# Kernel tuning notes

Measured on AMD Instinct MI355X. Metric: run time of the kernel, lower is better.

## Reference

```python
import jax, jax.numpy as jnp
import numpy as np
import math


def setup_inputs() -> dict:
    key = jax.random.key(0)
    k1, k2, k3 = jax.random.split(key, 3)
    B, L, H, E = 2, 2048, 8, 64
    queries = jax.random.normal(k1, (B, L, H, E), dtype=jnp.float32)
    keys = jax.random.normal(k2, (B, L, H, E), dtype=jnp.float32)
    values = jax.random.normal(k3, (B, L, H, E), dtype=jnp.float32)
    return {"queries": queries, "keys": keys, "values": values}


def reference(queries, keys, values):
    B, L, H, E = queries.shape
    scale = 1.0 / math.sqrt(E)
    # [B,H,L,S] attention scores
    scores = jnp.einsum('blhe,bshe->bhls', queries, keys)
    # causal mask: positions s > l masked to -inf (scale * -inf stays -inf)
    causal = jnp.triu(jnp.ones((L, L), dtype=bool), k=1)  # True above diagonal
    scores = jnp.where(causal[None, None, :, :], -jnp.inf, scores)
    attn = scale * scores
    SA = jax.nn.softmax(attn, axis=-1)  # dropout p=0.0 -> identity
    V = jnp.einsum('bhls,bshd->blhd', SA, values)
    return (V, SA)
```

## Files before the change

### kernel.cpp

```cpp
#include <hip/hip_runtime.h>
#include <math.h>

#define L_DIM 2048
#define H_DIM 8
#define ROWSTRIDE 512
#define NT 512
#define QSCALE 0.18033688011112042f

typedef __attribute__((ext_vector_type(8))) short short8;
typedef __attribute__((ext_vector_type(4))) float floatx4;

__device__ __forceinline__ unsigned short f2bf(float f) {
    unsigned int u = __builtin_bit_cast(unsigned int, f);
    return (unsigned short)((u + 0x8000u) >> 16);
}

__device__ __forceinline__ float fexp2(float x) {
#if __has_builtin(__builtin_amdgcn_exp2f)
    return __builtin_amdgcn_exp2f(x);
#else
    return exp2f(x);
#endif
}

__global__ __launch_bounds__(NT, 4)
void attn_mfma2(const float* __restrict__ Q, const float* __restrict__ K,
                const float* __restrict__ Vv, float* __restrict__ outV,
                float* __restrict__ outSA)
{
    __shared__ __align__(16) unsigned char smem[65536];
    unsigned short* Qs = (unsigned short*)(smem);
    unsigned short* Ks = (unsigned short*)(smem + 9216);
    unsigned short* Vt = (unsigned short*)(smem + 27648);
    unsigned short* Ps = (unsigned short*)(smem + 46080);
    float* Ml = (float*)(smem + 64512);
    float* Ll = (float*)(smem + 65024);
    float* Ob = (float*)(smem + 9216);

    const int t   = threadIdx.x;
    const int g   = t >> 8;
    const int u   = t & 255;
    const int bid = blockIdx.x;
    const int idx = bid & 31;
    const int qt  = (idx & 1) ? (31 - (idx >> 1)) : (idx >> 1);
    const int bh  = bid >> 5;
    const int h   = bh & 7;
    const int b   = bh >> 3;
    const int q0  = qt << 6;

    const int lane = t & 63;
    const int wg   = (t >> 6) & 3;
    const int l15  = lane & 15;
    const int quad = lane >> 4;

    const float* Qb = Q  + (size_t)b * L_DIM * ROWSTRIDE + h * 64;
    const float* Kb = K  + (size_t)b * L_DIM * ROWSTRIDE + h * 64;
    const float* Vb = Vv + (size_t)b * L_DIM * ROWSTRIDE + h * 64;
    float* saBase = outSA + (size_t)(b * H_DIM + h) * L_DIM * L_DIM;

    {
        const int sr = t >> 3, se = (t & 7) * 8;
        const float* src = Qb + (size_t)(q0 + sr) * ROWSTRIDE + se;
        float4 f0 = *(const float4*)(src);
        float4 f1 = *(const float4*)(src + 4);
        union { unsigned short us[8]; short8 v; } p;
        p.us[0] = f2bf(f0.x * QSCALE); p.us[1] = f2bf(f0.y * QSCALE);
        p.us[2] = f2bf(f0.z * QSCALE); p.us[3] = f2bf(f0.w * QSCALE);
        p.us[4] = f2bf(f1.x * QSCALE); p.us[5] = f2bf(f1.y * QSCALE);
        p.us[6] = f2bf(f1.z * QSCALE); p.us[7] = f2bf(f1.w * QSCALE);
        *(short8*)&Qs[sr * 72 + se] = p.v;
    }
    __syncthreads();

    const short8 aQ0 = *(const short8*)&Qs[(16 * wg + l15) * 72 + quad * 8];
    const short8 aQ1 = *(const short8*)&Qs[(16 * wg + l15) * 72 + 32 + quad * 8];

    const int ntiles = qt + 1;
    const int niter  = (ntiles + 1) >> 1;
    const int ksr = u >> 2, kse = (u & 3) * 16;
    unsigned short* myKs = Ks + g * 4608;
    unsigned short* myVt = Vt + g * 4608;
    unsigned short* myPs = Ps + g * 4608;

    float m_r[4], l_r[4];
#pragma unroll
    for (int r = 0; r < 4; ++r) { m_r[r] = -INFINITY; l_r[r] = 0.f; }

    for (int it = 0; it < niter; ++it) {
        const int st = 2 * it + g;
        const bool active = (st < ntiles);
        const int s0 = st << 6;
        __syncthreads();
        if (active) {
            const float* src = Kb + (size_t)(s0 + ksr) * ROWSTRIDE + kse;
            float4 f0 = *(const float4*)(src + 0);
            float4 f1 = *(const float4*)(src + 4);
            float4 f2 = *(const float4*)(src + 8);
            float4 f3 = *(const float4*)(src + 12);
            union { unsigned short us[8]; short8 v; } p0, p1;
            p0.us[0]=f2bf(f0.x); p0.us[1]=f2bf(f0.y); p0.us[2]=f2bf(f0.z); p0.us[3]=f2bf(f0.w);
            p0.us[4]=f2bf(f1.x); p0.us[5]=f2bf(f1.y); p0.us[6]=f2bf(f1.z); p0.us[7]=f2bf(f1.w);
            p1.us[0]=f2bf(f2.x); p1.us[1]=f2bf(f2.y); p1.us[2]=f2bf(f2.z); p1.us[3]=f2bf(f2.w);
            p1.us[4]=f2bf(f3.x); p1.us[5]=f2bf(f3.y); p1.us[6]=f2bf(f3.z); p1.us[7]=f2bf(f3.w);
            *(short8*)&myKs[ksr * 72 + kse]     = p0.v;
            *(short8*)&myKs[ksr * 72 + kse + 8] = p1.v;
        }
        __syncthreads();
        if (!active) continue;

        floatx4 d[4];
#pragma unroll
        for (int j = 0; j < 4; ++j) {
            short8 b0 = *(const short8*)&myKs[(16 * j + l15) * 72 + quad * 8];
            short8 b1 = *(const short8*)&myKs[(16 * j + l15) * 72 + 32 + quad * 8];
            floatx4 acc = {0.f, 0.f, 0.f, 0.f};
            acc = __builtin_amdgcn_mfma_f32_16x16x32_bf16(aQ0, b0, acc, 0, 0, 0);
            acc = __builtin_amdgcn_mfma_f32_16x16x32_bf16(aQ1, b1, acc, 0, 0, 0);
            d[j] = acc;
        }
        const bool diag = (st == qt);
#pragma unroll
        for (int r = 0; r < 4; ++r) {
            const int lrow = q0 + 16 * wg + quad * 4 + r;
            float v0 = d[0][r], v1 = d[1][r], v2 = d[2][r], v3 = d[3][r];
            if (diag) {
                v0 = (s0 +  0 + l15 <= lrow) ? v0 : -INFINITY;
                v1 = (s0 + 16 + l15 <= lrow) ? v1 : -INFINITY;
                v2 = (s0 + 32 + l15 <= lrow) ? v2 : -INFINITY;
                v3 = (s0 + 48 + l15 <= lrow) ? v3 : -INFINITY;
            }
            float vm = fmaxf(fmaxf(v0, v1), fmaxf(v2, v3));
#pragma unroll
            for (int mk = 1; mk < 16; mk <<= 1) vm = fmaxf(vm, __shfl_xor(vm, mk));
            const float mnew = fmaxf(m_r[r], vm);
            float es = fexp2(v0 - mnew) + fexp2(v1 - mnew) +
                       fexp2(v2 - mnew) + fexp2(v3 - mnew);
#pragma unroll
            for (int mk = 1; mk < 16; mk <<= 1) es += __shfl_xor(es, mk);
            l_r[r] = l_r[r] * fexp2(m_r[r] - mnew) + es;
            m_r[r] = mnew;
        }
    }

    __syncthreads();
    if (l15 == 0) {
#pragma unroll
        for (int r = 0; r < 4; ++r) {
            const int row = 16 * wg + quad * 4 + r;
            Ml[g * 64 + row] = m_r[r];
            Ll[g * 64 + row] = l_r[r];
        }
    }
    __syncthreads();
    float mfin[4], invl[4];
#pragma unroll
    for (int r = 0; r < 4; ++r) {
        const int row = 16 * wg + quad * 4 + r;
        float m0 = Ml[row], m1 = Ml[64 + row];
        float l0 = Ll[row], l1 = Ll[64 + row];
        float mf = fmaxf(m0, m1);
        float lf = l0 * fexp2(m0 - mf) + l1 * fexp2(m1 - mf);
        mfin[r] = mf;
        invl[r] = 1.0f / lf;
    }

    floatx4 oacc[4];
#pragma unroll
    for (int j = 0; j < 4; ++j) oacc[j] = (floatx4){0.f, 0.f, 0.f, 0.f};

    for (int it = 0; it < niter; ++it) {
        const int st = 2 * it + g;
        const bool active = (st < ntiles);
        const int s0 = st << 6;
        __syncthreads();
        if (active) {
            {
                const float* src = Kb + (size_t)(s0 + ksr) * ROWSTRIDE + kse;
                float4 f0 = *(const float4*)(src + 0);
                float4 f1 = *(const float4*)(src + 4);
                float4 f2 = *(const float4*)(src + 8);
                float4 f3 = *(const float4*)(src + 12);
                union { unsigned short us[8]; short8 v; } p0, p1;
                p0.us[0]=f2bf(f0.x); p0.us[1]=f2bf(f0.y); p0.us[2]=f2bf(f0.z); p0.us[3]=f2bf(f0.w);
                p0.us[4]=f2bf(f1.x); p0.us[5]=f2bf(f1.y); p0.us[6]=f2bf(f1.z); p0.us[7]=f2bf(f1.w);
                p1.us[0]=f2bf(f2.x); p1.us[1]=f2bf(f2.y); p1.us[2]=f2bf(f2.z); p1.us[3]=f2bf(f2.w);
                p1.us[4]=f2bf(f3.x); p1.us[5]=f2bf(f3.y); p1.us[6]=f2bf(f3.z); p1.us[7]=f2bf(f3.w);
                *(short8*)&myKs[ksr * 72 + kse]     = p0.v;
                *(short8*)&myKs[ksr * 72 + kse + 8] = p1.v;
            }
            {
                const float* src = Vb + (size_t)(s0 + ksr) * ROWSTRIDE + kse;
                float4 f0 = *(const float4*)(src + 0);
                float4 f1 = *(const float4*)(src + 4);
                float4 f2 = *(const float4*)(src + 8);
                float4 f3 = *(const float4*)(src + 12);
                myVt[(kse +  0) * 72 + ksr] = f2bf(f0.x);
                myVt[(kse +  1) * 72 + ksr] = f2bf(f0.y);
                myVt[(kse +  2) * 72 + ksr] = f2bf(f0.z);
                myVt[(kse +  3) * 72 + ksr] = f2bf(f0.w);
                myVt[(kse +  4) * 72 + ksr] = f2bf(f1.x);
                myVt[(kse +  5) * 72 + ksr] = f2bf(f1.y);
                myVt[(kse +  6) * 72 + ksr] = f2bf(f1.z);
                myVt[(kse +  7) * 72 + ksr] = f2bf(f1.w);
                myVt[(kse +  8) * 72 + ksr] = f2bf(f2.x);
                myVt[(kse +  9) * 72 + ksr] = f2bf(f2.y);
                myVt[(kse + 10) * 72 + ksr] = f2bf(f2.z);
                myVt[(kse + 11) * 72 + ksr] = f2bf(f2.w);
                myVt[(kse + 12) * 72 + ksr] = f2bf(f3.x);
                myVt[(kse + 13) * 72 + ksr] = f2bf(f3.y);
                myVt[(kse + 14) * 72 + ksr] = f2bf(f3.z);
                myVt[(kse + 15) * 72 + ksr] = f2bf(f3.w);
            }
        }
        __syncthreads();
        if (!active) continue;

        floatx4 d[4];
#pragma unroll
        for (int j = 0; j < 4; ++j) {
            short8 b0 = *(const short8*)&myKs[(16 * j + l15) * 72 + quad * 8];
            short8 b1 = *(const short8*)&myKs[(16 * j + l15) * 72 + 32 + quad * 8];
            floatx4 acc = {0.f, 0.f, 0.f, 0.f};
            acc = __builtin_amdgcn_mfma_f32_16x16x32_bf16(aQ0, b0, acc, 0, 0, 0);
            acc = __builtin_amdgcn_mfma_f32_16x16x32_bf16(aQ1, b1, acc, 0, 0, 0);
            d[j] = acc;
        }
        const bool diag = (st == qt);
#pragma unroll
        for (int r = 0; r < 4; ++r) {
            const int lrow = q0 + 16 * wg + quad * 4 + r;
            float* sap = saBase + (size_t)lrow * L_DIM + s0 + l15;
            const float mr = mfin[r], il = invl[r];
#pragma unroll
            for (int j = 0; j < 4; ++j) {
                float v = d[j][r];
                bool ok = !diag || (s0 + 16 * j + l15 <= lrow);
                float p = ok ? fexp2(v - mr) * il : 0.0f;
                sap[16 * j] = p;
                myPs[(16 * wg + quad * 4 + r) * 72 + 16 * j + l15] = f2bf(p);
            }
        }
        short8 aP0 = *(const short8*)&myPs[(16 * wg + l15) * 72 + quad * 8];
        short8 aP1 = *(const short8*)&myPs[(16 * wg + l15) * 72 + 32 + quad * 8];
#pragma unroll
        for (int j = 0; j < 4; ++j) {
            short8 bv0 = *(const short8*)&myVt[(16 * j + l15) * 72 + quad * 8];
            short8 bv1 = *(const short8*)&myVt[(16 * j + l15) * 72 + 32 + quad * 8];
            oacc[j] = __builtin_amdgcn_mfma_f32_16x16x32_bf16(aP0, bv0, oacc[j], 0, 0, 0);
            oacc[j] = __builtin_amdgcn_mfma_f32_16x16x32_bf16(aP1, bv1, oacc[j], 0, 0, 0);
        }
    }

    __syncthreads();
    if (g == 1) {
#pragma unroll
        for (int r = 0; r < 4; ++r) {
            const int row = 16 * wg + quad * 4 + r;
#pragma unroll
            for (int j = 0; j < 4; ++j)
                Ob[row * 65 + 16 * j + l15] = oacc[j][r];
        }
    }
    __syncthreads();
    if (g == 0) {
#pragma unroll
        for (int r = 0; r < 4; ++r) {
            const int row = 16 * wg + quad * 4 + r;
            float* op = outV + ((size_t)b * L_DIM + q0 + row) * ROWSTRIDE + h * 64 + l15;
#pragma unroll
            for (int j = 0; j < 4; ++j)
                op[16 * j] = oacc[j][r] + Ob[row * 65 + 16 * j + l15];
        }
    }

    {
        const int z0 = ntiles << 6;
        const int zr = t >> 3;
        float* rowp = saBase + (size_t)(q0 + zr) * L_DIM;
        const float4 zf = {0.f, 0.f, 0.f, 0.f};
        for (int s = z0 + (t & 7) * 4; s < L_DIM; s += 32)
            *(float4*)(rowp + s) = zf;
    }
}

extern "C" void kernel_launch(void* const* d_in, const int* in_sizes, int n_in,
                              void* d_out, int out_size, void* d_ws, size_t ws_size,
                              hipStream_t stream) {
    const float* Q  = (const float*)d_in[0];
    const float* K  = (const float*)d_in[1];
    const float* Vv = (const float*)d_in[2];
    float* out   = (float*)d_out;
    float* outV  = out;
    float* outSA = out + (size_t)2 * L_DIM * H_DIM * 64;

    dim3 grid(2 * H_DIM * 32);
    dim3 block(NT);
    attn_mfma2<<<grid, block, 0, stream>>>(Q, K, Vv, outV, outSA);
}
```

Before: 388.7 us.

## Pair causal query tiles per block, load K directly, double-buffer swizzled V

Each block now handles two query tiles (qt and 31-qt), which balances causal work and halves the grid to 256 blocks. Q and K fragments are loaded straight from global memory into MFMA registers, so there is no K staging in shared memory. V is transposed into a swizzled double buffer, and the next tile is prefetched while the current one computes, which removes one barrier per iteration. In exchange, register pressure rises (launch bounds drop to 2 blocks per SM), the direct K loads are less coalesced, and K is read twice from global memory.

```diff
diff --git a/kernel.cpp b/kernel.cpp
--- a/kernel.cpp
+++ b/kernel.cpp
@@ -23,263 +23,271 @@
 #endif
 }
 
-__global__ __launch_bounds__(NT, 4)
-void attn_mfma2(const float* __restrict__ Q, const float* __restrict__ K,
+__device__ __forceinline__ short8 pack8(float4 a, float4 b) {
+    union { unsigned short us[8]; short8 v; } pk;
+    pk.us[0]=f2bf(a.x); pk.us[1]=f2bf(a.y); pk.us[2]=f2bf(a.z); pk.us[3]=f2bf(a.w);
+    pk.us[4]=f2bf(b.x); pk.us[5]=f2bf(b.y); pk.us[6]=f2bf(b.z); pk.us[7]=f2bf(b.w);
+    return pk.v;
+}
+
+__device__ __forceinline__ short8 pack8q(float4 a, float4 b) {
+    union { unsigned short us[8]; short8 v; } pk;
+    pk.us[0]=f2bf(a.x*QSCALE); pk.us[1]=f2bf(a.y*QSCALE);
+    pk.us[2]=f2bf(a.z*QSCALE); pk.us[3]=f2bf(a.w*QSCALE);
+    pk.us[4]=f2bf(b.x*QSCALE); pk.us[5]=f2bf(b.y*QSCALE);
+    pk.us[6]=f2bf(b.z*QSCALE); pk.us[7]=f2bf(b.w*QSCALE);
+    return pk.v;
+}
+
+__global__ __launch_bounds__(NT, 2)
+void attn_mfma3(const float* __restrict__ Q, const float* __restrict__ K,
                 const float* __restrict__ Vv, float* __restrict__ outV,
                 float* __restrict__ outSA)
 {
-    __shared__ __align__(16) unsigned char smem[65536];
-    unsigned short* Qs = (unsigned short*)(smem);
-    unsigned short* Ks = (unsigned short*)(smem + 9216);
-    unsigned short* Vt = (unsigned short*)(smem + 27648);
-    unsigned short* Ps = (unsigned short*)(smem + 46080);
-    float* Ml = (float*)(smem + 64512);
-    float* Ll = (float*)(smem + 65024);
-    float* Ob = (float*)(smem + 9216);
+    __shared__ __align__(16) unsigned char smem[56320];
+    unsigned short* Vt = (unsigned short*)(smem);
+    unsigned short* Ps = (unsigned short*)(smem + 36864);
+    float* Ml = (float*)(smem + 55296);
+    float* Ll = (float*)(smem + 55808);
+    float* Ob = (float*)(smem);
 
     const int t   = threadIdx.x;
     const int g   = t >> 8;
     const int u   = t & 255;
     const int bid = blockIdx.x;
-    const int idx = bid & 31;
-    const int qt  = (idx & 1) ? (31 - (idx >> 1)) : (idx >> 1);
-    const int bh  = bid >> 5;
+    const int bh  = bid & 15;
+    const int pp  = bid >> 4;
     const int h   = bh & 7;
     const int b   = bh >> 3;
-    const int q0  = qt << 6;
 
     const int lane = t & 63;
     const int wg   = (t >> 6) & 3;
     const int l15  = lane & 15;
     const int quad = lane >> 4;
 
+    const int ksr = u >> 2, kse = (u & 3) * 16;
+    const int vswz = ksr ^ (kse >> 1);
+
     const float* Qb = Q  + (size_t)b * L_DIM * ROWSTRIDE + h * 64;
     const float* Kb = K  + (size_t)b * L_DIM * ROWSTRIDE + h * 64;
     const float* Vb = Vv + (size_t)b * L_DIM * ROWSTRIDE + h * 64;
     float* saBase = outSA + (size_t)(b * H_DIM + h) * L_DIM * L_DIM;
 
-    {
-        const int sr = t >> 3, se = (t & 7) * 8;
-        const float* src = Qb + (size_t)(q0 + sr) * ROWSTRIDE + se;
-        float4 f0 = *(const float4*)(src);
-        float4 f1 = *(const float4*)(src + 4);
-        union { unsigned short us[8]; short8 v; } p;
-        p.us[0] = f2bf(f0.x * QSCALE); p.us[1] = f2bf(f0.y * QSCALE);
-        p.us[2] = f2bf(f0.z * QSCALE); p.us[3] = f2bf(f0.w * QSCALE);
-        p.us[4] = f2bf(f1.x * QSCALE); p.us[5] = f2bf(f1.y * QSCALE);
-        p.us[6] = f2bf(f1.z * QSCALE); p.us[7] = f2bf(f1.w * QSCALE);
-        *(short8*)&Qs[sr * 72 + se] = p.v;
-    }
-    __syncthreads();
-
-    const short8 aQ0 = *(const short8*)&Qs[(16 * wg + l15) * 72 + quad * 8];
-    const short8 aQ1 = *(const short8*)&Qs[(16 * wg + l15) * 72 + 32 + quad * 8];
-
-    const int ntiles = qt + 1;
-    const int niter  = (ntiles + 1) >> 1;
-    const int ksr = u >> 2, kse = (u & 3) * 16;
-    unsigned short* myKs = Ks + g * 4608;
-    unsigned short* myVt = Vt + g * 4608;
+    unsigned short* myVt = Vt + g * 9216;
     unsigned short* myPs = Ps + g * 4608;
 
-    float m_r[4], l_r[4];
-#pragma unroll
-    for (int r = 0; r < 4; ++r) { m_r[r] = -INFINITY; l_r[r] = 0.f; }
-
-    for (int it = 0; it < niter; ++it) {
-        const int st = 2 * it + g;
-        const bool active = (st < ntiles);
-        const int s0 = st << 6;
+    for (int qsel = 0; qsel < 2; ++qsel) {
+        const int qt = qsel ? pp : (31 - pp);
+        const int q0 = qt << 6;
+        const int ntiles = qt + 1;
+        const int niter  = (ntiles + 1) >> 1;
+
+        short8 aQ0, aQ1;
+        {
+            const float* qsrc = Qb + (size_t)(q0 + 16 * wg + l15) * ROWSTRIDE + quad * 8;
+            aQ0 = pack8q(*(const float4*)(qsrc),      *(const float4*)(qsrc + 4));
+            aQ1 = pack8q(*(const float4*)(qsrc + 32), *(const float4*)(qsrc + 36));
+        }
+
+        float m_r[4], l_r[4];
+#pragma unroll
+        for (int r = 0; r < 4; ++r) { m_r[r] = -INFINITY; l_r[r] = 0.f; }
+
+        for (int st = g; st < ntiles; st += 2) {
+            const int s0 = st << 6;
+            const float* kbase = Kb + (size_t)(s0 + l15) * ROWSTRIDE + quad * 8;
+            float4 kr[16];
+#pragma unroll
+            for (int j = 0; j < 4; ++j) {
+                const float* kj = kbase + (size_t)(16 * j) * ROWSTRIDE;
+                kr[4*j+0] = *(const float4*)(kj);
+                kr[4*j+1] = *(const float4*)(kj + 4);
+                kr[4*j+2] = *(const float4*)(kj + 32);
+                kr[4*j+3] = *(const float4*)(kj + 36);
+            }
+            floatx4 d[4];
+#pragma unroll
+            for (int j = 0; j < 4; ++j) {
+                short8 b0 = pack8(kr[4*j+0], kr[4*j+1]);
+                short8 b1 = pack8(kr[4*j+2], kr[4*j+3]);
+                floatx4 acc = {0.f, 0.f, 0.f, 0.f};
+                acc = __builtin_amdgcn_mfma_f32_16x16x32_bf16(aQ0, b0, acc, 0, 0, 0);
+                acc = __builtin_amdgcn_mfma_f32_16x16x32_bf16(aQ1, b1, acc, 0, 0, 0);
+                d[j] = acc;
+            }
+            const bool diag = (st == qt);
+#pragma unroll
+            for (int r = 0; r < 4; ++r) {
+                const int lrow = q0 + 16 * wg + quad * 4 + r;
+                float v0 = d[0][r], v1 = d[1][r], v2 = d[2][r], v3 = d[3][r];
+                if (diag) {
+                    v0 = (s0 +  0 + l15 <= lrow) ? v0 : -INFINITY;
+                    v1 = (s0 + 16 + l15 <= lrow) ? v1 : -INFINITY;
+                    v2 = (s0 + 32 + l15 <= lrow) ? v2 : -INFINITY;
+                    v3 = (s0 + 48 + l15 <= lrow) ? v3 : -INFINITY;
+                }
+                float vm = fmaxf(fmaxf(v0, v1), fmaxf(v2, v3));
+#pragma unroll
+                for (int mk = 1; mk < 16; mk <<= 1) vm = fmaxf(vm, __shfl_xor(vm, mk));
+                const float mnew = fmaxf(m_r[r], vm);
+                float es = fexp2(v0 - mnew) + fexp2(v1 - mnew) +
+                           fexp2(v2 - mnew) + fexp2(v3 - mnew);
+#pragma unroll
+                for (int mk = 1; mk < 16; mk <<= 1) es += __shfl_xor(es, mk);
+                l_r[r] = l_r[r] * fexp2(m_r[r] - mnew) + es;
+                m_r[r] = mnew;
+            }
+        }
+
         __syncthreads();
-        if (active) {
-            const float* src = Kb + (size_t)(s0 + ksr) * ROWSTRIDE + kse;
-            float4 f0 = *(const float4*)(src + 0);
+        if (l15 == 0) {
+#pragma unroll
+            for (int r = 0; r < 4; ++r) {
+                const int row = 16 * wg + quad * 4 + r;
+                Ml[g * 64 + row] = m_r[r];
+                Ll[g * 64 + row] = l_r[r];
+            }
+        }
+        __syncthreads();
+        float mfin[4], invl[4];
+#pragma unroll
+        for (int r = 0; r < 4; ++r) {
+            const int row = 16 * wg + quad * 4 + r;
+            float m0 = Ml[row], m1 = Ml[64 + row];
+            float l0 = Ll[row], l1 = Ll[64 + row];
+            float mf = fmaxf(m0, m1);
+            float lf = l0 * fexp2(m0 - mf) + l1 * fexp2(m1 - mf);
+            mfin[r] = mf;
+            invl[r] = 1.0f / lf;
+        }
+
+        floatx4 oacc[4];
+#pragma unroll
+        for (int j = 0; j < 4; ++j) oacc[j] = (floatx4){0.f, 0.f, 0.f, 0.f};
+
+        if (g < ntiles) {
+            const float* src = Vb + (size_t)((g << 6) + ksr) * ROWSTRIDE + kse;
+            float4 f0 = *(const float4*)(src);
             float4 f1 = *(const float4*)(src + 4);
             float4 f2 = *(const float4*)(src + 8);
             float4 f3 = *(const float4*)(src + 12);
-            union { unsigned short us[8]; short8 v; } p0, p1;
-            p0.us[0]=f2bf(f0.x); p0.us[1]=f2bf(f0.y); p0.us[2]=f2bf(f0.z); p0.us[3]=f2bf(f0.w);
-            p0.us[4]=f2bf(f1.x); p0.us[5]=f2bf(f1.y); p0.us[6]=f2bf(f1.z); p0.us[7]=f2bf(f1.w);
-            p1.us[0]=f2bf(f2.x); p1.us[1]=f2bf(f2.y); p1.us[2]=f2bf(f2.z); p1.us[3]=f2bf(f2.w);
-            p1.us[4]=f2bf(f3.x); p1.us[5]=f2bf(f3.y); p1.us[6]=f2bf(f3.z); p1.us[7]=f2bf(f3.w);
-            *(short8*)&myKs[ksr * 72 + kse]     = p0.v;
-            *(short8*)&myKs[ksr * 72 + kse + 8] = p1.v;
+            unsigned short* vtw = myVt + vswz;
+            vtw[(kse+ 0)*72] = f2bf(f0.x); vtw[(kse+ 1)*72] = f2bf(f0.y);
+            vtw[(kse+ 2)*72] = f2bf(f0.z); vtw[(kse+ 3)*72] = f2bf(f0.w);
+            vtw[(kse+ 4)*72] = f2bf(f1.x); vtw[(kse+ 5)*72] = f2bf(f1.y);
+            vtw[(kse+ 6)*72] = f2bf(f1.z); vtw[(kse+ 7)*72] = f2bf(f1.w);
+            vtw[(kse+ 8)*72] = f2bf(f2.x); vtw[(kse+ 9)*72] = f2bf(f2.y);
+            vtw[(kse+10)*72] = f2bf(f2.z); vtw[(kse+11)*72] = f2bf(f2.w);
+            vtw[(kse+12)*72] = f2bf(f3.x); vtw[(kse+13)*72] = f2bf(f3.y);
+            vtw[(kse+14)*72] = f2bf(f3.z); vtw[(kse+15)*72] = f2bf(f3.w);
         }
         __syncthreads();
-        if (!active) continue;
-
-        floatx4 d[4];
-#pragma unroll
-        for (int j = 0; j < 4; ++j) {
-            short8 b0 = *(const short8*)&myKs[(16 * j + l15) * 72 + quad * 8];
-            short8 b1 = *(const short8*)&myKs[(16 * j + l15) * 72 + 32 + quad * 8];
-            floatx4 acc = {0.f, 0.f, 0.f, 0.f};
-            acc = __builtin_amdgcn_mfma_f32_16x16x32_bf16(aQ0, b0, acc, 0, 0, 0);
-            acc = __builtin_amdgcn_mfma_f32_16x16x32_bf16(aQ1, b1, acc, 0, 0, 0);
-            d[j] = acc;
-        }
-        const bool diag = (st == qt);
-#pragma unroll
-        for (int r = 0; r < 4; ++r) {
-            const int lrow = q0 + 16 * wg + quad * 4 + r;
-            float v0 = d[0][r], v1 = d[1][r], v2 = d[2][r], v3 = d[3][r];
-            if (diag) {
-                v0 = (s0 +  0 + l15 <= lrow) ? v0 : -INFINITY;
-                v1 = (s0 + 16 + l15 <= lrow) ? v1 : -INFINITY;
-                v2 = (s0 + 32 + l15 <= lrow) ? v2 : -INFINITY;
-                v3 = (s0 + 48 + l15 <= lrow) ? v3 : -INFINITY;
-            }
-            float vm = fmaxf(fmaxf(v0, v1), fmaxf(v2, v3));
-#pragma unroll
-            for (int mk = 1; mk < 16; mk <<= 1) vm = fmaxf(vm, __shfl_xor(vm, mk));
-            const float mnew = fmaxf(m_r[r], vm);
-            float es = fexp2(v0 - mnew) + fexp2(v1 - mnew) +
-                       fexp2(v2 - mnew) + fexp2(v3 - mnew);
-#pragma unroll
-            for (int mk = 1; mk < 16; mk <<= 1) es += __shfl_xor(es, mk);
-            l_r[r] = l_r[r] * fexp2(m_r[r] - mnew) + es;
-            m_r[r] = mnew;
-        }
-    }
-
-    __syncthreads();
-    if (l15 == 0) {
-#pragma unroll
-        for (int r = 0; r < 4; ++r) {
-            const int row = 16 * wg + quad * 4 + r;
-            Ml[g * 64 + row] = m_r[r];
-            Ll[g * 64 + row] = l_r[r];
-        }
-    }
-    __syncthreads();
-    float mfin[4], invl[4];
-#pragma unroll
-    for (int r = 0; r < 4; ++r) {
-        const int row = 16 * wg + quad * 4 + r;
-        float m0 = Ml[row], m1 = Ml[64 + row];
-        float l0 = Ll[row], l1 = Ll[64 + row];
-        float mf = fmaxf(m0, m1);
-        float lf = l0 * fexp2(m0 - mf) + l1 * fexp2(m1 - mf);
-        mfin[r] = mf;
-        invl[r] = 1.0f / lf;
-    }
-
-    floatx4 oacc[4];
-#pragma unroll
-    for (int j = 0; j < 4; ++j) oacc[j] = (floatx4){0.f, 0.f, 0.f, 0.f};
-
-    for (int it = 0; it < niter; ++it) {
-        const int st = 2 * it + g;
-        const bool active = (st < ntiles);
-        const int s0 = st << 6;
+
+        for (int it = 0; it < niter; ++it) {
+            const int st = 2 * it + g;
+            const bool active = (st < ntiles);
+            const int stn = st + 2;
+            const bool nact = (stn < ntiles);
+            const int stc = nact ? stn : (ntiles - 1);
+            const float* vsrc = Vb + (size_t)((stc << 6) + ksr) * ROWSTRIDE + kse;
+            float4 f0 = *(const float4*)(vsrc);
+            float4 f1 = *(const float4*)(vsrc + 4);
+            float4 f2 = *(const float4*)(vsrc + 8);
+            float4 f3 = *(const float4*)(vsrc + 12);
+
+            if (active) {
+                const int s0 = st << 6;
+                const float* kbase = Kb + (size_t)(s0 + l15) * ROWSTRIDE + quad * 8;
+                float4 kr[16];
+#pragma unroll
+                for (int j = 0; j < 4; ++j) {
+                    const float* kj = kbase + (size_t)(16 * j) * ROWSTRIDE;
+                    kr[4*j+0] = *(const float4*)(kj);
+                    kr[4*j+1] = *(const float4*)(kj + 4);
+                    kr[4*j+2] = *(const float4*)(kj + 32);
+                    kr[4*j+3] = *(const float4*)(kj + 36);
+                }
+                floatx4 d[4];
+#pragma unroll
+                for (int j = 0; j < 4; ++j) {
+                    short8 b0 = pack8(kr[4*j+0], kr[4*j+1]);
+                    short8 b1 = pack8(kr[4*j+2], kr[4*j+3]);
+                    floatx4 acc = {0.f, 0.f, 0.f, 0.f};
+                    acc = __builtin_amdgcn_mfma_f32_16x16x32_bf16(aQ0, b0, acc, 0, 0, 0);
+                    acc = __builtin_amdgcn_mfma_f32_16x16x32_bf16(aQ1, b1, acc, 0, 0, 0);
+                    d[j] = acc;
+                }
+                const bool diag = (st == qt);
+#pragma unroll
+                for (int r = 0; r < 4; ++r) {
+                    const int lrow = q0 + 16 * wg + quad * 4 + r;
+                    float* sap = saBase + (size_t)lrow * L_DIM + s0 + l15;
+                    const float mr = mfin[r], il = invl[r];
+#pragma unroll
+                    for (int j = 0; j < 4; ++j) {
+                        float v = d[j][r];
+                        bool ok = !diag || (s0 + 16 * j + l15 <= lrow);
+                        float p = ok ? fexp2(v - mr) * il : 0.0f;
+                        sap[16 * j] = p;
+                        myPs[(16 * wg + quad * 4 + r) * 72 + 16 * j + l15] = f2bf(p);
+                    }
+                }
+                short8 aP0 = *(const short8*)&myPs[(16 * wg + l15) * 72 + quad * 8];
+                short8 aP1 = *(const short8*)&myPs[(16 * wg + l15) * 72 + 32 + quad * 8];
+                const unsigned short* vtr = myVt + (it & 1) * 4608;
+#pragma unroll
+                for (int j = 0; j < 4; ++j) {
+                    const unsigned short* vb = vtr + (16 * j + l15) * 72;
+                    short8 bv0 = *(const short8*)&vb[(quad ^ j) * 8];
+                    short8 bv1 = *(const short8*)&vb[32 + (quad ^ j) * 8];
+                    oacc[j] = __builtin_amdgcn_mfma_f32_16x16x32_bf16(aP0, bv0, oacc[j], 0, 0, 0);
+                    oacc[j] = __builtin_amdgcn_mfma_f32_16x16x32_bf16(aP1, bv1, oacc[j], 0, 0, 0);
+                }
+            }
+
+            if (nact) {
+                unsigned short* vtw = myVt + ((it + 1) & 1) * 4608 + vswz;
+                vtw[(kse+ 0)*72] = f2bf(f0.x); vtw[(kse+ 1)*72] = f2bf(f0.y);
+                vtw[(kse+ 2)*72] = f2bf(f0.z); vtw[(kse+ 3)*72] = f2bf(f0.w);
+                vtw[(kse+ 4)*72] = f2bf(f1.x); vtw[(kse+ 5)*72] = f2bf(f1.y);
+                vtw[(kse+ 6)*72] = f2bf(f1.z); vtw[(kse+ 7)*72] = f2bf(f1.w);
+                vtw[(kse+ 8)*72] = f2bf(f2.x); vtw[(kse+ 9)*72] = f2bf(f2.y);
+                vtw[(kse+10)*72] = f2bf(f2.z); vtw[(kse+11)*72] = f2bf(f2.w);
+                vtw[(kse+12)*72] = f2bf(f3.x); vtw[(kse+13)*72] = f2bf(f3.y);
+                vtw[(kse+14)*72] = f2bf(f3.z); vtw[(kse+15)*72] = f2bf(f3.w);
+            }
+            __syncthreads();
+        }
+
+        if (g == 1) {
+#pragma unroll
+            for (int r = 0; r < 4; ++r) {
+                const int row = 16 * wg + quad * 4 + r;
+#pragma unroll
+                for (int j = 0; j < 4; ++j)
+                    Ob[row * 65 + 16 * j + l15] = oacc[j][r];
+            }
+        }
         __syncthreads();
-        if (active) {
-            {
-                const float* src = Kb + (size_t)(s0 + ksr) * ROWSTRIDE + kse;
-                float4 f0 = *(const float4*)(src + 0);
-                float4 f1 = *(const float4*)(src + 4);
-                float4 f2 = *(const float4*)(src + 8);
-                float4 f3 = *(const float4*)(src + 12);
-                union { unsigned short us[8]; short8 v; } p0, p1;
-                p0.us[0]=f2bf(f0.x); p0.us[1]=f2bf(f0.y); p0.us[2]=f2bf(f0.z); p0.us[3]=f2bf(f0.w);
-                p0.us[4]=f2bf(f1.x); p0.us[5]=f2bf(f1.y); p0.us[6]=f2bf(f1.z); p0.us[7]=f2bf(f1.w);
-                p1.us[0]=f2bf(f2.x); p1.us[1]=f2bf(f2.y); p1.us[2]=f2bf(f2.z); p1.us[3]=f2bf(f2.w);
-                p1.us[4]=f2bf(f3.x); p1.us[5]=f2bf(f3.y); p1.us[6]=f2bf(f3.z); p1.us[7]=f2bf(f3.w);
-                *(short8*)&myKs[ksr * 72 + kse]     = p0.v;
-                *(short8*)&myKs[ksr * 72 + kse + 8] = p1.v;
-            }
-            {
-                const float* src = Vb + (size_t)(s0 + ksr) * ROWSTRIDE + kse;
-                float4 f0 = *(const float4*)(src + 0);
-                float4 f1 = *(const float4*)(src + 4);
-                float4 f2 = *(const float4*)(src + 8);
-                float4 f3 = *(const float4*)(src + 12);
-                myVt[(kse +  0) * 72 + ksr] = f2bf(f0.x);
-                myVt[(kse +  1) * 72 + ksr] = f2bf(f0.y);
-                myVt[(kse +  2) * 72 + ksr] = f2bf(f0.z);
-                myVt[(kse +  3) * 72 + ksr] = f2bf(f0.w);
-                myVt[(kse +  4) * 72 + ksr] = f2bf(f1.x);
-                myVt[(kse +  5) * 72 + ksr] = f2bf(f1.y);
-                myVt[(kse +  6) * 72 + ksr] = f2bf(f1.z);
-                myVt[(kse +  7) * 72 + ksr] = f2bf(f1.w);
-                myVt[(kse +  8) * 72 + ksr] = f2bf(f2.x);
-                myVt[(kse +  9) * 72 + ksr] = f2bf(f2.y);
-                myVt[(kse + 10) * 72 + ksr] = f2bf(f2.z);
-                myVt[(kse + 11) * 72 + ksr] = f2bf(f2.w);
-                myVt[(kse + 12) * 72 + ksr] = f2bf(f3.x);
-                myVt[(kse + 13) * 72 + ksr] = f2bf(f3.y);
-                myVt[(kse + 14) * 72 + ksr] = f2bf(f3.z);
-                myVt[(kse + 15) * 72 + ksr] = f2bf(f3.w);
-            }
-        }
-        __syncthreads();
-        if (!active) continue;
-
-        floatx4 d[4];
-#pragma unroll
-        for (int j = 0; j < 4; ++j) {
-            short8 b0 = *(const short8*)&myKs[(16 * j + l15) * 72 + quad * 8];
-            short8 b1 = *(const short8*)&myKs[(16 * j + l15) * 72 + 32 + quad * 8];
-            floatx4 acc = {0.f, 0.f, 0.f, 0.f};
-            acc = __builtin_amdgcn_mfma_f32_16x16x32_bf16(aQ0, b0, acc, 0, 0, 0);
-            acc = __builtin_amdgcn_mfma_f32_16x16x32_bf16(aQ1, b1, acc, 0, 0, 0);
-            d[j] = acc;
-        }
-        const bool diag = (st == qt);
-#pragma unroll
-        for (int r = 0; r < 4; ++r) {
-            const int lrow = q0 + 16 * wg + quad * 4 + r;
-            float* sap = saBase + (size_t)lrow * L_DIM + s0 + l15;
-            const float mr = mfin[r], il = invl[r];
-#pragma unroll
-            for (int j = 0; j < 4; ++j) {
-                float v = d[j][r];
-                bool ok = !diag || (s0 + 16 * j + l15 <= lrow);
-                float p = ok ? fexp2(v - mr) * il : 0.0f;
-                sap[16 * j] = p;
-                myPs[(16 * wg + quad * 4 + r) * 72 + 16 * j + l15] = f2bf(p);
-            }
-        }
-        short8 aP0 = *(const short8*)&myPs[(16 * wg + l15) * 72 + quad * 8];
-        short8 aP1 = *(const short8*)&myPs[(16 * wg + l15) * 72 + 32 + quad * 8];
-#pragma unroll
-        for (int j = 0; j < 4; ++j) {
-            short8 bv0 = *(const short8*)&myVt[(16 * j + l15) * 72 + quad * 8];
-            short8 bv1 = *(const short8*)&myVt[(16 * j + l15) * 72 + 32 + quad * 8];
-            oacc[j] = __builtin_amdgcn_mfma_f32_16x16x32_bf16(aP0, bv0, oacc[j], 0, 0, 0);
-            oacc[j] = __builtin_amdgcn_mfma_f32_16x16x32_bf16(aP1, bv1, oacc[j], 0, 0, 0);
-        }
-    }
-
-    __syncthreads();
-    if (g == 1) {
-#pragma unroll
-        for (int r = 0; r < 4; ++r) {
-            const int row = 16 * wg + quad * 4 + r;
-#pragma unroll
-            for (int j = 0; j < 4; ++j)
-                Ob[row * 65 + 16 * j + l15] = oacc[j][r];
-        }
-    }
-    __syncthreads();
-    if (g == 0) {
-#pragma unroll
-        for (int r = 0; r < 4; ++r) {
-            const int row = 16 * wg + quad * 4 + r;
-            float* op = outV + ((size_t)b * L_DIM + q0 + row) * ROWSTRIDE + h * 64 + l15;
-#pragma unroll
-            for (int j = 0; j < 4; ++j)
-                op[16 * j] = oacc[j][r] + Ob[row * 65 + 16 * j + l15];
-        }
-    }
-
-    {
-        const int z0 = ntiles << 6;
-        const int zr = t >> 3;
-        float* rowp = saBase + (size_t)(q0 + zr) * L_DIM;
-        const float4 zf = {0.f, 0.f, 0.f, 0.f};
-        for (int s = z0 + (t & 7) * 4; s < L_DIM; s += 32)
-            *(float4*)(rowp + s) = zf;
+        if (g == 0) {
+#pragma unroll
+            for (int r = 0; r < 4; ++r) {
+                const int row = 16 * wg + quad * 4 + r;
+                float* op = outV + ((size_t)b * L_DIM + q0 + row) * ROWSTRIDE + h * 64 + l15;
+#pragma unroll
+                for (int j = 0; j < 4; ++j)
+                    op[16 * j] = oacc[j][r] + Ob[row * 65 + 16 * j + l15];
+            }
+        }
+
+        {
+            const int z0 = ntiles << 6;
+            const int zr = t >> 3;
+            float* rowp = saBase + (size_t)(q0 + zr) * L_DIM;
+            const float4 zf = {0.f, 0.f, 0.f, 0.f};
+            for (int s = z0 + (t & 7) * 4; s < L_DIM; s += 32)
+                *(float4*)(rowp + s) = zf;
+        }
     }
 }
 
@@ -293,7 +301,7 @@
     float* outV  = out;
     float* outSA = out + (size_t)2 * L_DIM * H_DIM * 64;
 
-    dim3 grid(2 * H_DIM * 32);
+    dim3 grid(256);
     dim3 block(NT);
-    attn_mfma2<<<grid, block, 0, stream>>>(Q, K, Vv, outV, outSA);
-}
+    attn_mfma3<<<grid, block, 0, stream>>>(Q, K, Vv, outV, outSA);
+}
```

Result: slower. 426.8 us (+9.8%).
